# Optimization experiments

Hardware: AMD Instinct MI355X
Metric: run time of the kernel (lower is better)

Reference implementation:

```python
import jax, jax.numpy as jnp
import numpy as np

GRID = 16  # int(sqrt(num_patches=256))
# fixed ragged grid shapes: 32 images cycling through 4 aspect ratios
_SHAPES = np.array([[32, 32], [16, 64], [24, 40], [40, 24]] * 8, dtype=np.int64)  # [32,2]
_SIZES = _SHAPES[:, 0] * _SHAPES[:, 1]  # per-image patch counts
_SEQ_LEN = int(_SIZES.sum())  # 31744


def setup_inputs() -> dict:
    key = jax.random.key(0)
    k1, k2, k3 = jax.random.split(key, 3)
    return {
        "seq_patches": jax.random.normal(k1, (_SEQ_LEN, 768), dtype=jnp.float32),
        "w": jax.random.normal(k2, (1152, 768), dtype=jnp.float32) * 0.02,
        "b": jnp.zeros((1152,), dtype=jnp.float32),
        "pos_emb": jax.random.normal(k3, (256, 1152), dtype=jnp.float32) * 0.02,
        "seq_sizes": jnp.asarray(_SIZES),
        "spatial_shapes": jnp.asarray(_SHAPES),
    }


def reference(seq_patches, w, b, pos_emb, seq_sizes, spatial_shapes):
    # Linear patch embedding: [S, 768] @ [768, 1152] + [1152]
    patch_embeds = seq_patches @ w.T + b
    d = pos_emb.shape[-1]
    pos_grid = pos_emb.reshape(GRID, GRID, d)  # [16,16,D]
    shapes = np.asarray(spatial_shapes)  # static host-side shapes (ragged loop)
    pos_list = []
    for h, wd in shapes:
        # antialiased bilinear resize, half-pixel centers (align_corners=False)
        rp = jax.image.resize(pos_grid, (int(h), int(wd), d), method="linear", antialias=True)
        pos_list.append(rp.reshape(int(h) * int(wd), d))
    pos_embeds = jnp.concatenate(pos_list, axis=0)  # [S, D]
    return patch_embeds + pos_embeds
```

## Files before the change

### kernel.cpp

```cpp
#include <hip/hip_runtime.h>
#include <hip/hip_bf16.h>
#include <cstdint>
#include <cstddef>

typedef __attribute__((ext_vector_type(8))) short short8;
typedef __attribute__((ext_vector_type(4))) float f32x4;

static constexpr int M_TOT = 31744;
static constexpr int N_TOT = 1152;
static constexpr int K_TOT = 768;
static constexpr long A_ELEMS = (long)M_TOT * K_TOT;
static constexpr long W_ELEMS = (long)N_TOT * K_TOT;
static constexpr int CYC_ROWS = 3968;

__device__ __forceinline__ unsigned short f2bf(float f) {
  unsigned int u = __float_as_uint(f);
  u += 0x7FFFu + ((u >> 16) & 1u);
  return (unsigned short)(u >> 16);
}
__device__ __forceinline__ float bf2f(unsigned short u) {
  return __uint_as_float((unsigned int)u << 16);
}

__global__ void cvt_kernel(const float* __restrict__ A, const float* __restrict__ W,
                           unsigned short* __restrict__ dst) {
  long chunk = (long)blockIdx.x * blockDim.x + threadIdx.x;
  long i = chunk * 8;
  const float* src = (i < A_ELEMS) ? (A + i) : (W + (i - A_ELEMS));
  float4 v0 = *(const float4*)(src);
  float4 v1 = *(const float4*)(src + 4);
  short8 o;
  o[0] = (short)f2bf(v0.x); o[1] = (short)f2bf(v0.y);
  o[2] = (short)f2bf(v0.z); o[3] = (short)f2bf(v0.w);
  o[4] = (short)f2bf(v1.x); o[5] = (short)f2bf(v1.y);
  o[6] = (short)f2bf(v1.z); o[7] = (short)f2bf(v1.w);
  *(short8*)(dst + i) = o;
}

__global__ void tab_kernel(const float* __restrict__ pos, const float* __restrict__ bias,
                           unsigned short* __restrict__ tab) {
  const int t = blockIdx.x * blockDim.x + threadIdx.x;
  const int row = t / 144;
  const int dc = (t - row * 144) * 8;

  int rr, cc; float sy, sx;
  if (row < 1024)      { rr = row >> 5; cc = row & 31; sy = 0.5f;         sx = 0.5f; }
  else if (row < 2048) { const int li = row - 1024; rr = li >> 6; cc = li & 63; sy = 1.0f; sx = 0.25f; }
  else if (row < 3008) { const int li = row - 2048; rr = li / 40; cc = li - rr * 40; sy = 16.0f / 24.0f; sx = 0.4f; }
  else                 { const int li = row - 3008; rr = li / 24; cc = li - rr * 24; sy = 0.4f; sx = 16.0f / 24.0f; }
  float yc = fminf(fmaxf(((float)rr + 0.5f) * sy - 0.5f, 0.0f), 15.0f);
  const int y0 = (int)yc; const float fy = yc - (float)y0;
  const int y1 = y0 < 15 ? y0 + 1 : 15;
  float xc = fminf(fmaxf(((float)cc + 0.5f) * sx - 0.5f, 0.0f), 15.0f);
  const int x0 = (int)xc; const float fx = xc - (float)x0;
  const int x1 = x0 < 15 ? x0 + 1 : 15;
  const float w11 = fy * fx;
  const float w10 = fy - w11;
  const float w01 = fx - w11;
  const float w00 = 1.0f - fy - fx + w11;
  const float* p00 = pos + (size_t)(y0 * 16 + x0) * 1152 + dc;
  const float* p01 = pos + (size_t)(y0 * 16 + x1) * 1152 + dc;
  const float* p10 = pos + (size_t)(y1 * 16 + x0) * 1152 + dc;
  const float* p11 = pos + (size_t)(y1 * 16 + x1) * 1152 + dc;
  const float* bi  = bias + dc;
  short8 o;
#pragma unroll
  for (int j = 0; j < 8; ++j) {
    const float v = bi[j] + w00 * p00[j] + w01 * p01[j] + w10 * p10[j] + w11 * p11[j];
    o[j] = (short)f2bf(v);
  }
  *(short8*)(tab + (size_t)row * 1152 + dc) = o;
}

__device__ __forceinline__ void gload_lds16(const void* g, void* l) {
  __builtin_amdgcn_global_load_lds((__attribute__((address_space(1))) void*)g,
                                   (__attribute__((address_space(3))) void*)l, 16, 0, 0);
}

__global__ __launch_bounds__(256) void gemm_kernel(
    const unsigned short* __restrict__ Abf, const unsigned short* __restrict__ Wbf,
    const unsigned short* __restrict__ tab, float* __restrict__ outp) {
  __shared__ __attribute__((aligned(16))) unsigned short As[128 * 64];
  __shared__ __attribute__((aligned(16))) unsigned short Bs[128 * 64];

  const int bid = blockIdx.x;
  const int tile = (bid & 7) * 279 + (bid >> 3);
  const int tm = tile / 9, tn = tile % 9;
  const int m0 = tm * 128, n0 = tn * 128;

  const int tid = threadIdx.x;
  const int wid = tid >> 6, lane = tid & 63;
  const int wr = wid >> 1, wc = wid & 1;
  const int rb = wid * 32;
  const int lrow = lane >> 3;
  const int lcol = ((lane & 7) ^ lrow) * 8;

  f32x4 acc[4][4] = {};

  const unsigned short* Abase = Abf + (size_t)m0 * K_TOT;
  const unsigned short* Bbase = Wbf + (size_t)n0 * K_TOT;

  for (int kt = 0; kt < 12; ++kt) {
    const int k0 = kt * 64;
#pragma unroll
    for (int c = 0; c < 4; ++c) {
      const int row = rb + c * 8;
      gload_lds16(Abase + (size_t)(row + lrow) * K_TOT + k0 + lcol,
                  (char*)As + row * 128);
      gload_lds16(Bbase + (size_t)(row + lrow) * K_TOT + k0 + lcol,
                  (char*)Bs + row * 128);
    }
    __syncthreads();

    const int kg = lane >> 4;
#pragma unroll
    for (int kk = 0; kk < 2; ++kk) {
      short8 fa[4], fb[4];
#pragma unroll
      for (int m = 0; m < 4; ++m) {
        const int arow = wr * 64 + m * 16 + (lane & 15);
        const int ab = arow * 128 + (((kk * 4 + kg) ^ (arow & 7)) << 4);
        fa[m] = *(const short8*)((const char*)As + ab);
      }
#pragma unroll
      for (int n = 0; n < 4; ++n) {
        const int brow = wc * 64 + n * 16 + (lane & 15);
        const int bb = brow * 128 + (((kk * 4 + kg) ^ (brow & 7)) << 4);
        fb[n] = *(const short8*)((const char*)Bs + bb);
      }
#pragma unroll
      for (int m = 0; m < 4; ++m)
#pragma unroll
        for (int n = 0; n < 4; ++n)
          acc[m][n] = __builtin_amdgcn_mfma_f32_16x16x32_bf16(fa[m], fb[n], acc[m][n], 0, 0, 0);
    }
    __syncthreads();
  }

  const int s_base = m0 + wr * 64 + ((lane >> 4) << 2);
  const int rem_base = s_base % CYC_ROWS;
  const int d_base = n0 + wc * 64 + (lane & 15);

#pragma unroll
  for (int m = 0; m < 4; ++m) {
#pragma unroll
    for (int r = 0; r < 4; ++r) {
      const int off = m * 16 + r;
      int rem = rem_base + off;
      if (rem >= CYC_ROWS) rem -= CYC_ROWS;
      const unsigned short* trow = tab + (size_t)rem * 1152 + d_base;
      float* orow = outp + (size_t)(s_base + off) * 1152 + d_base;
#pragma unroll
      for (int n = 0; n < 4; ++n)
        orow[n * 16] = acc[m][n][r] + bf2f(trow[n * 16]);
    }
  }
}

extern "C" void kernel_launch(void* const* d_in, const int* in_sizes, int n_in,
                              void* d_out, int out_size, void* d_ws, size_t ws_size,
                              hipStream_t stream) {
  const float* A    = (const float*)d_in[0];
  const float* W    = (const float*)d_in[1];
  const float* bias = (const float*)d_in[2];
  const float* pos  = (const float*)d_in[3];
  unsigned short* Abf = (unsigned short*)d_ws;
  unsigned short* Wbf = Abf + A_ELEMS;
  unsigned short* tab = Wbf + W_ELEMS;
  float* outp = (float*)d_out;

  cvt_kernel<<<12336, 256, 0, stream>>>(A, W, Abf);
  tab_kernel<<<2232, 256, 0, stream>>>(pos, bias, tab);
  gemm_kernel<<<2232, 256, 0, stream>>>(Abf, Wbf, tab, outp);
}
```

Measured before the change: 127.9 us.

## Rewrite GEMM as 256x256-tile, 8-wave, double-buffered pipelined kernel

The GEMM moves from 128x128 tiles with 4 waves and a single LDS buffer to 256x256 tiles with 8 waves. A/B stages are double-buffered and issued asynchronously, with explicit vmcnt waits, barriers and setprio around the MFMA groups so global loads overlap with matrix math. N=1152 is not a multiple of 256, so the last column tile clamps B rows and skips stores for out-of-range columns, which wastes some compute. The XCD-aware block remap is adjusted for the new 620-block grid.

```diff
diff --git a/kernel.cpp b/kernel.cpp
--- a/kernel.cpp
+++ b/kernel.cpp
@@ -77,82 +77,133 @@
                                    (__attribute__((address_space(3))) void*)l, 16, 0, 0);
 }
 
-__global__ __launch_bounds__(256) void gemm_kernel(
+__global__ __launch_bounds__(512, 2) void gemm_kernel(
     const unsigned short* __restrict__ Abf, const unsigned short* __restrict__ Wbf,
     const unsigned short* __restrict__ tab, float* __restrict__ outp) {
-  __shared__ __attribute__((aligned(16))) unsigned short As[128 * 64];
-  __shared__ __attribute__((aligned(16))) unsigned short Bs[128 * 64];
+  __shared__ __attribute__((aligned(16))) unsigned short As[2 * 2 * 256 * 32];
+  __shared__ __attribute__((aligned(16))) unsigned short Bs[2 * 2 * 256 * 32];
 
   const int bid = blockIdx.x;
-  const int tile = (bid & 7) * 279 + (bid >> 3);
-  const int tm = tile / 9, tn = tile % 9;
-  const int m0 = tm * 128, n0 = tn * 128;
+  const int xcd = bid & 7, idx = bid >> 3;
+  const int wgid = (xcd < 4 ? xcd * 78 : 312 + (xcd - 4) * 77) + idx;
+  const int tm = wgid / 5, tn = wgid - tm * 5;
+  const int m0 = tm * 256, n0 = tn * 256;
 
   const int tid = threadIdx.x;
-  const int wid = tid >> 6, lane = tid & 63;
-  const int wr = wid >> 1, wc = wid & 1;
-  const int rb = wid * 32;
-  const int lrow = lane >> 3;
-  const int lcol = ((lane & 7) ^ lrow) * 8;
-
-  f32x4 acc[4][4] = {};
-
-  const unsigned short* Abase = Abf + (size_t)m0 * K_TOT;
-  const unsigned short* Bbase = Wbf + (size_t)n0 * K_TOT;
-
-  for (int kt = 0; kt < 12; ++kt) {
-    const int k0 = kt * 64;
-#pragma unroll
-    for (int c = 0; c < 4; ++c) {
-      const int row = rb + c * 8;
-      gload_lds16(Abase + (size_t)(row + lrow) * K_TOT + k0 + lcol,
-                  (char*)As + row * 128);
-      gload_lds16(Bbase + (size_t)(row + lrow) * K_TOT + k0 + lcol,
-                  (char*)Bs + row * 128);
-    }
-    __syncthreads();
-
-    const int kg = lane >> 4;
-#pragma unroll
-    for (int kk = 0; kk < 2; ++kk) {
-      short8 fa[4], fb[4];
-#pragma unroll
-      for (int m = 0; m < 4; ++m) {
-        const int arow = wr * 64 + m * 16 + (lane & 15);
-        const int ab = arow * 128 + (((kk * 4 + kg) ^ (arow & 7)) << 4);
-        fa[m] = *(const short8*)((const char*)As + ab);
+  const int w = tid >> 6, lane = tid & 63;
+  const int wm = w >> 2, wn = w & 3;
+  const int kg = lane >> 4, l15 = lane & 15;
+  const int rkey = (l15 >> 1) & 3;
+
+  const int srow = lane >> 2;
+  const int csrc = ((lane & 3) ^ ((lane >> 3) & 3)) * 8;
+  const int sdst = w * 2048;
+
+  const unsigned short* ApA = Abf + (size_t)(m0 + w * 32 + srow) * K_TOT + csrc;
+  int brow0 = n0 + w * 32 + srow;      if (brow0 > N_TOT - 1) brow0 = N_TOT - 1;
+  int brow1 = n0 + w * 32 + 16 + srow; if (brow1 > N_TOT - 1) brow1 = N_TOT - 1;
+  const unsigned short* BpB0 = Wbf + (size_t)brow0 * K_TOT + csrc;
+  const unsigned short* BpB1 = Wbf + (size_t)brow1 * K_TOT + csrc;
+
+  f32x4 acc[8][4] = {};
+  short8 fa[4], fb[4];
+
+#define UOFF(p_, kk_) (((p_) * 2 + (kk_)) << 14)
+
+#define STAGE_A(p_, kk_, kt_)                                                    \
+  { const unsigned short* s_ = ApA + (kt_) * 64 + (kk_) * 32;                    \
+    gload_lds16(s_, (char*)As + UOFF(p_, kk_) + sdst);                           \
+    gload_lds16(s_ + (size_t)16 * K_TOT, (char*)As + UOFF(p_, kk_) + sdst + 1024); }
+
+#define STAGE_B(p_, kk_, kt_)                                                    \
+  { gload_lds16(BpB0 + (kt_) * 64 + (kk_) * 32, (char*)Bs + UOFF(p_, kk_) + sdst); \
+    gload_lds16(BpB1 + (kt_) * 64 + (kk_) * 32, (char*)Bs + UOFF(p_, kk_) + sdst + 1024); }
+
+#define LOAD_FA(p_, kk_, s_)                                                     \
+  _Pragma("unroll") for (int j = 0; j < 4; ++j) {                                \
+    const int ar_ = wm * 128 + (s_) * 64 + j * 16 + l15;                         \
+    fa[j] = *(const short8*)((const char*)As + UOFF(p_, kk_) + ar_ * 64 +        \
+                             ((kg ^ rkey) << 4));                                \
+  }
+
+#define LOAD_FB(p_, kk_)                                                         \
+  _Pragma("unroll") for (int n = 0; n < 4; ++n) {                                \
+    const int br_ = wn * 64 + n * 16 + l15;                                      \
+    fb[n] = *(const short8*)((const char*)Bs + UOFF(p_, kk_) + br_ * 64 +        \
+                             ((kg ^ rkey) << 4));                                \
+  }
+
+#define MFMA16(s_)                                                               \
+  _Pragma("unroll") for (int j = 0; j < 4; ++j)                                  \
+    _Pragma("unroll") for (int n = 0; n < 4; ++n)                                \
+      acc[(s_) * 4 + j][n] = __builtin_amdgcn_mfma_f32_16x16x32_bf16(            \
+          fa[j], fb[n], acc[(s_) * 4 + j][n], 0, 0, 0);
+
+#define BAR __builtin_amdgcn_s_barrier()
+#define SP1 __builtin_amdgcn_s_setprio(1)
+#define SP0 __builtin_amdgcn_s_setprio(0)
+
+  STAGE_B(0, 0, 0)
+  STAGE_A(0, 0, 0)
+  STAGE_B(0, 1, 0)
+  STAGE_A(0, 1, 0)
+  STAGE_B(1, 0, 1)
+  STAGE_A(1, 0, 1)
+  STAGE_B(1, 1, 1)
+  asm volatile("s_waitcnt vmcnt(8)" ::: "memory");
+  BAR;
+
+#pragma unroll
+  for (int t = 0; t < 12; ++t) {
+    const int p = t & 1, q = p ^ 1;
+    LOAD_FB(p, 0)
+    LOAD_FA(p, 0, 0)
+    if (t + 1 <= 11) STAGE_A(q, 1, t + 1)
+    BAR; SP1; MFMA16(0) SP0;
+    BAR;
+    LOAD_FA(p, 0, 1)
+    if (t + 2 <= 11) STAGE_B(p, 0, t + 2)
+    BAR; SP1; MFMA16(1) SP0;
+    if (t <= 9)       { asm volatile("s_waitcnt vmcnt(10)" ::: "memory"); }
+    else if (t == 10) { asm volatile("s_waitcnt vmcnt(8)"  ::: "memory"); }
+    else              { asm volatile("s_waitcnt vmcnt(0)"  ::: "memory"); }
+    BAR;
+    LOAD_FB(p, 1)
+    LOAD_FA(p, 1, 0)
+    if (t + 2 <= 11) STAGE_A(p, 0, t + 2)
+    BAR; SP1; MFMA16(0) SP0;
+    BAR;
+    LOAD_FA(p, 1, 1)
+    if (t + 2 <= 11) STAGE_B(p, 1, t + 2)
+    BAR; SP1; MFMA16(1) SP0;
+    if (t <= 9)       { asm volatile("s_waitcnt vmcnt(8)" ::: "memory"); BAR; }
+    else if (t == 10) { asm volatile("s_waitcnt vmcnt(4)" ::: "memory"); BAR; }
+  }
+
+#undef STAGE_A
+#undef STAGE_B
+#undef LOAD_FA
+#undef LOAD_FB
+#undef MFMA16
+#undef UOFF
+
+  const int d_base = n0 + wn * 64 + l15;
+  if (d_base < N_TOT) {
+    const int s_base = m0 + wm * 128 + ((lane >> 4) << 2);
+    const int rem_b = s_base % CYC_ROWS;
+#pragma unroll
+    for (int i = 0; i < 8; ++i) {
+      const int roff = ((i >> 2) << 6) + ((i & 3) << 4);
+#pragma unroll
+      for (int r = 0; r < 4; ++r) {
+        int rem = rem_b + roff + r;
+        if (rem >= CYC_ROWS) rem -= CYC_ROWS;
+        const unsigned short* trow = tab + (size_t)rem * 1152 + d_base;
+        float* orow = outp + (size_t)(s_base + roff + r) * 1152 + d_base;
+#pragma unroll
+        for (int n = 0; n < 4; ++n)
+          orow[n * 16] = acc[i][n][r] + bf2f(trow[n * 16]);
       }
-#pragma unroll
-      for (int n = 0; n < 4; ++n) {
-        const int brow = wc * 64 + n * 16 + (lane & 15);
-        const int bb = brow * 128 + (((kk * 4 + kg) ^ (brow & 7)) << 4);
-        fb[n] = *(const short8*)((const char*)Bs + bb);
-      }
-#pragma unroll
-      for (int m = 0; m < 4; ++m)
-#pragma unroll
-        for (int n = 0; n < 4; ++n)
-          acc[m][n] = __builtin_amdgcn_mfma_f32_16x16x32_bf16(fa[m], fb[n], acc[m][n], 0, 0, 0);
-    }
-    __syncthreads();
-  }
-
-  const int s_base = m0 + wr * 64 + ((lane >> 4) << 2);
-  const int rem_base = s_base % CYC_ROWS;
-  const int d_base = n0 + wc * 64 + (lane & 15);
-
-#pragma unroll
-  for (int m = 0; m < 4; ++m) {
-#pragma unroll
-    for (int r = 0; r < 4; ++r) {
-      const int off = m * 16 + r;
-      int rem = rem_base + off;
-      if (rem >= CYC_ROWS) rem -= CYC_ROWS;
-      const unsigned short* trow = tab + (size_t)rem * 1152 + d_base;
-      float* orow = outp + (size_t)(s_base + off) * 1152 + d_base;
-#pragma unroll
-      for (int n = 0; n < 4; ++n)
-        orow[n * 16] = acc[m][n][r] + bf2f(trow[n * 16]);
     }
   }
 }
@@ -171,5 +222,5 @@
 
   cvt_kernel<<<12336, 256, 0, stream>>>(A, W, Abf);
   tab_kernel<<<2232, 256, 0, stream>>>(pos, bias, tab);
-  gemm_kernel<<<2232, 256, 0, stream>>>(Abf, Wbf, tab, outp);
-}
+  gemm_kernel<<<620, 512, 0, stream>>>(Abf, Wbf, tab, outp);
+}
```

New measurement: 135.4 us. 5.9% more time.

## Load GEMM MFMA fragments directly from global memory, dropping LDS staging

Applied to the files above, without the earlier changes.

The GEMM kernel no longer stages A and B tiles through shared memory with global_load_lds and barriers. Each lane now loads its MFMA operand fragments straight from global memory into registers, and the fully unrolled K loop raises wave priority around the MFMA blocks. This removes the LDS round trip and the per-tile __syncthreads, and sets launch bounds for 3 blocks per CU. In exchange, waves sharing rows or columns now issue redundant global and L2 traffic, the loads use a strided 16-byte-per-lane pattern with poorer coalescing, and register pressure rises.

```diff
diff --git a/kernel.cpp b/kernel.cpp
--- a/kernel.cpp
+++ b/kernel.cpp
@@ -72,17 +72,9 @@
   *(short8*)(tab + (size_t)row * 1152 + dc) = o;
 }
 
-__device__ __forceinline__ void gload_lds16(const void* g, void* l) {
-  __builtin_amdgcn_global_load_lds((__attribute__((address_space(1))) void*)g,
-                                   (__attribute__((address_space(3))) void*)l, 16, 0, 0);
-}
-
-__global__ __launch_bounds__(256) void gemm_kernel(
+__global__ __launch_bounds__(256, 3) void gemm_kernel(
     const unsigned short* __restrict__ Abf, const unsigned short* __restrict__ Wbf,
     const unsigned short* __restrict__ tab, float* __restrict__ outp) {
-  __shared__ __attribute__((aligned(16))) unsigned short As[128 * 64];
-  __shared__ __attribute__((aligned(16))) unsigned short Bs[128 * 64];
-
   const int bid = blockIdx.x;
   const int tile = (bid & 7) * 279 + (bid >> 3);
   const int tm = tile / 9, tn = tile % 9;
@@ -91,55 +83,48 @@
   const int tid = threadIdx.x;
   const int wid = tid >> 6, lane = tid & 63;
   const int wr = wid >> 1, wc = wid & 1;
-  const int rb = wid * 32;
-  const int lrow = lane >> 3;
-  const int lcol = ((lane & 7) ^ lrow) * 8;
+  const int kg = lane >> 4, l15 = lane & 15;
+
+  const unsigned short* Ab[4];
+  const unsigned short* Bb[4];
+#pragma unroll
+  for (int m = 0; m < 4; ++m)
+    Ab[m] = Abf + (size_t)(m0 + wr * 64 + m * 16 + l15) * K_TOT + kg * 8;
+#pragma unroll
+  for (int n = 0; n < 4; ++n)
+    Bb[n] = Wbf + (size_t)(n0 + wc * 64 + n * 16 + l15) * K_TOT + kg * 8;
 
   f32x4 acc[4][4] = {};
 
-  const unsigned short* Abase = Abf + (size_t)m0 * K_TOT;
-  const unsigned short* Bbase = Wbf + (size_t)n0 * K_TOT;
-
-  for (int kt = 0; kt < 12; ++kt) {
-    const int k0 = kt * 64;
 #pragma unroll
-    for (int c = 0; c < 4; ++c) {
-      const int row = rb + c * 8;
-      gload_lds16(Abase + (size_t)(row + lrow) * K_TOT + k0 + lcol,
-                  (char*)As + row * 128);
-      gload_lds16(Bbase + (size_t)(row + lrow) * K_TOT + k0 + lcol,
-                  (char*)Bs + row * 128);
-    }
-    __syncthreads();
-
-    const int kg = lane >> 4;
+  for (int t = 0; t < 12; ++t) {
+    const int ko = t * 64;
+    short8 fa0[4], fb0[4], fa1[4], fb1[4];
 #pragma unroll
-    for (int kk = 0; kk < 2; ++kk) {
-      short8 fa[4], fb[4];
+    for (int n = 0; n < 4; ++n) fb0[n] = *(const short8*)(Bb[n] + ko);
 #pragma unroll
-      for (int m = 0; m < 4; ++m) {
-        const int arow = wr * 64 + m * 16 + (lane & 15);
-        const int ab = arow * 128 + (((kk * 4 + kg) ^ (arow & 7)) << 4);
-        fa[m] = *(const short8*)((const char*)As + ab);
-      }
+    for (int m = 0; m < 4; ++m) fa0[m] = *(const short8*)(Ab[m] + ko);
 #pragma unroll
-      for (int n = 0; n < 4; ++n) {
-        const int brow = wc * 64 + n * 16 + (lane & 15);
-        const int bb = brow * 128 + (((kk * 4 + kg) ^ (brow & 7)) << 4);
-        fb[n] = *(const short8*)((const char*)Bs + bb);
-      }
+    for (int n = 0; n < 4; ++n) fb1[n] = *(const short8*)(Bb[n] + ko + 32);
 #pragma unroll
-      for (int m = 0; m < 4; ++m)
+    for (int m = 0; m < 4; ++m) fa1[m] = *(const short8*)(Ab[m] + ko + 32);
+    __builtin_amdgcn_s_setprio(1);
 #pragma unroll
-        for (int n = 0; n < 4; ++n)
-          acc[m][n] = __builtin_amdgcn_mfma_f32_16x16x32_bf16(fa[m], fb[n], acc[m][n], 0, 0, 0);
-    }
-    __syncthreads();
+    for (int m = 0; m < 4; ++m)
+#pragma unroll
+      for (int n = 0; n < 4; ++n)
+        acc[m][n] = __builtin_amdgcn_mfma_f32_16x16x32_bf16(fa0[m], fb0[n], acc[m][n], 0, 0, 0);
+#pragma unroll
+    for (int m = 0; m < 4; ++m)
+#pragma unroll
+      for (int n = 0; n < 4; ++n)
+        acc[m][n] = __builtin_amdgcn_mfma_f32_16x16x32_bf16(fa1[m], fb1[n], acc[m][n], 0, 0, 0);
+    __builtin_amdgcn_s_setprio(0);
   }
 
   const int s_base = m0 + wr * 64 + ((lane >> 4) << 2);
   const int rem_base = s_base % CYC_ROWS;
-  const int d_base = n0 + wc * 64 + (lane & 15);
+  const int d_base = n0 + wc * 64 + l15;
 
 #pragma unroll
   for (int m = 0; m < 4; ++m) {
```

Result: slower. 238.4 us (+86.4%).
